# Performance work log

Measured on AMD Instinct MI355X. Metric: run time of the kernel, lower is better.

Reference implementation:

```python
import jax, jax.numpy as jnp
import numpy as np

D = 1024
H = 16
B = 8
N = 1024


def setup_inputs() -> dict:
    key = jax.random.key(0)
    k1, k2, k3 = jax.random.split(key, 3)
    x = jax.random.normal(k1, (B, N, D), dtype=jnp.float32)
    w_in = jax.random.normal(k2, (D, 3 * D), dtype=jnp.float32) * (1.0 / np.sqrt(D))
    w_out = jax.random.normal(k3, (D, D), dtype=jnp.float32) * (1.0 / np.sqrt(D))
    b_out = jnp.zeros((D,), dtype=jnp.float32)
    return {"x": x, "w_in": w_in, "w_out": w_out, "b_out": b_out}


def reference(x, w_in, w_out, b_out):
    h = H
    d = D // H
    scale = D ** (-0.5)  # note: full dimension, per source
    qkv = x @ w_in  # [B, N, 3D]
    # rearrange 'b n (qkv h d) -> qkv b h n d'
    qkv = qkv.reshape(x.shape[0], x.shape[1], 3, h, d)
    qkv = jnp.transpose(qkv, (2, 0, 3, 1, 4))
    q, k, v = qkv[0], qkv[1], qkv[2]
    scores = jnp.einsum('bhid,bhjd->bhij', q, k) * scale
    attn = jax.nn.softmax(scores, axis=-1)
    out = jnp.einsum('bhij,bhjd->bhid', attn, v)
    # 'b h n d -> b n (h d)'
    out = jnp.transpose(out, (0, 2, 1, 3)).reshape(x.shape[0], x.shape[1], h * d)
    return out @ w_out + b_out
```

## Files before the change

kernel.cpp:

```cpp
#include <hip/hip_runtime.h>
#include <stdint.h>
#include <stddef.h>

typedef __bf16 bf16;
typedef __bf16 bf16x4 __attribute__((ext_vector_type(4)));
typedef __bf16 bf16x8 __attribute__((ext_vector_type(8)));
typedef float  f32x4  __attribute__((ext_vector_type(4)));
typedef float  f32x16 __attribute__((ext_vector_type(16)));
typedef float  f32x4v __attribute__((ext_vector_type(4)));
typedef unsigned int u32x4 __attribute__((ext_vector_type(4)));

__device__ __forceinline__ void gload_lds16(const void* g, void* lds) {
  __builtin_amdgcn_global_load_lds(
      (__attribute__((address_space(1))) void*)(uintptr_t)g,
      (__attribute__((address_space(3))) void*)lds,
      16, 0, 0);
}

__device__ __forceinline__ unsigned int pk2(float a, float b) {
  unsigned short lo = __builtin_bit_cast(unsigned short, (bf16)a);
  unsigned short hi = __builtin_bit_cast(unsigned short, (bf16)b);
  return (unsigned int)lo | ((unsigned int)hi << 16);
}


__global__ void cvt_f32_to_bf16(const float* __restrict__ in, bf16* __restrict__ out, int n) {
  int i = (blockIdx.x * blockDim.x + threadIdx.x) * 4;
  if (i >= n) return;
  f32x4v v = *reinterpret_cast<const f32x4v*>(in + i);
  bf16x4 o;
  o[0] = (bf16)v[0]; o[1] = (bf16)v[1]; o[2] = (bf16)v[2]; o[3] = (bf16)v[3];
  *reinterpret_cast<bf16x4*>(out + i) = o;
}

__global__ void transpose_cvt(const float* __restrict__ in, bf16* __restrict__ out, int R, int C) {
  __shared__ bf16 tile[32][33];
  int c0 = blockIdx.x * 32, r0 = blockIdx.y * 32;
  int tx = threadIdx.x, ty = threadIdx.y;
  #pragma unroll
  for (int i = ty; i < 32; i += 8)
    tile[i][tx] = (bf16)in[(size_t)(r0 + i) * C + (c0 + tx)];
  __syncthreads();
  #pragma unroll
  for (int i = ty; i < 32; i += 8)
    out[(size_t)(c0 + i) * R + (r0 + tx)] = tile[tx][i];
}


template <typename OT, bool BIAS>
__global__ __launch_bounds__(256) void gemm_abt(
    const bf16* __restrict__ A,
    const bf16* __restrict__ Bt,
    const float* __restrict__ bias,
    OT* __restrict__ C, int M, int N, int K)
{
  __shared__ bf16 As[128 * 64];
  __shared__ bf16 Bs[128 * 64];

  const int tid = threadIdx.x;
  const int w = tid >> 6, l = tid & 63;
  const int l15 = l & 15, l4 = l >> 4, l7 = l & 7;
  const int wr = w >> 1, wc = w & 1;
  const int m0 = blockIdx.y * 128, n0 = blockIdx.x * 128;

  f32x4 acc[4][4];
  #pragma unroll
  for (int i = 0; i < 4; i++)
    #pragma unroll
    for (int j = 0; j < 4; j++) acc[i][j] = (f32x4){0.f, 0.f, 0.f, 0.f};

  const int srow  = w * 8 + (l >> 3);
  const int sslot = (l & 7) ^ ((l >> 3) & 7);
  const int KT = K >> 6;

  for (int kt = 0; kt < KT; ++kt) {
    __syncthreads();
    const int kcol = kt * 64 + sslot * 8;
    #pragma unroll
    for (int p = 0; p < 4; ++p) {
      gload_lds16(A  + (size_t)(m0 + p * 32 + srow) * K + kcol,
                  (char*)As + p * 4096 + w * 1024);
      gload_lds16(Bt + (size_t)(n0 + p * 32 + srow) * K + kcol,
                  (char*)Bs + p * 4096 + w * 1024);
    }
    __syncthreads();

    #pragma unroll
    for (int kk = 0; kk < 2; ++kk) {
      const int coff = (kk * 32 + l4 * 8) ^ (l7 << 3);
      bf16x8 af[4], bq[4];
      #pragma unroll
      for (int m = 0; m < 4; ++m) {
        int r = wr * 64 + m * 16 + l15;
        af[m] = *reinterpret_cast<const bf16x8*>(&As[r * 64 + coff]);
      }
      #pragma unroll
      for (int n = 0; n < 4; ++n) {
        int r = wc * 64 + n * 16 + l15;
        bq[n] = *reinterpret_cast<const bf16x8*>(&Bs[r * 64 + coff]);
      }
      #pragma unroll
      for (int m = 0; m < 4; ++m)
        #pragma unroll
        for (int n = 0; n < 4; ++n)
          acc[m][n] = __builtin_amdgcn_mfma_f32_16x16x32_bf16(af[m], bq[n], acc[m][n], 0, 0, 0);
    }
  }

  #pragma unroll
  for (int m = 0; m < 4; ++m) {
    #pragma unroll
    for (int n = 0; n < 4; ++n) {
      int col = n0 + wc * 64 + n * 16 + l15;
      float bv = BIAS ? bias[col] : 0.f;
      #pragma unroll
      for (int j = 0; j < 4; ++j) {
        int row = m0 + wr * 64 + m * 16 + l4 * 4 + j;
        float v = acc[m][n][j] + bv;
        C[(size_t)row * N + col] = (OT)v;
      }
    }
  }
}


__global__ __launch_bounds__(256) void attn_fused(
    const bf16* __restrict__ qkv,
    bf16* __restrict__ aout)
{
  __shared__ bf16 Ks[64 * 64];
  __shared__ bf16 Vt[64 * 64];

  const int tid = threadIdx.x;
  const int w = tid >> 6, l = tid & 63;
  const int l31 = l & 31, hi = l >> 5;

  const int bid = blockIdx.x;
  const int c  = bid & 7, rr = bid >> 3;
  const int g  = c * 16 + (rr & 15);
  const int qt = rr >> 4;
  const int h  = g & 15;
  const int b  = g >> 4;

  const bf16* base = qkv + (size_t)b * 1024 * 3072;
  const int qrow0 = qt * 128 + w * 32;

  const float qscale = 0.03125f * 1.44269504f;
  bf16x8 qf[4];
  #pragma unroll
  for (int st = 0; st < 4; st++) {
    const bf16* p = base + (size_t)(qrow0 + l31) * 3072 + h * 64 + st * 16 + hi * 8;
    bf16x8 v = *reinterpret_cast<const bf16x8*>(p);
    #pragma unroll
    for (int e = 0; e < 8; e++) v[e] = (bf16)((float)v[e] * qscale);
    qf[st] = v;
  }

  bf16x8 onesf;
  #pragma unroll
  for (int e = 0; e < 8; e++) onesf[e] = (bf16)1.0f;

  f32x16 acc0 = {}, acc1 = {}, accS = {};

  const int skey  = w * 8 + (l >> 3);
  const int sslot = (l & 7) ^ ((l >> 3) & 7);
  const int vd0   = (tid & 15) * 4;
  const int vk0   = (tid >> 4) * 4;
  const int vslot = tid >> 5;
  const int vhalf = (tid >> 4) & 1;

  for (int kt = 0; kt < 16; ++kt) {
    __syncthreads();
    #pragma unroll
    for (int p = 0; p < 2; ++p)
      gload_lds16(base + (size_t)(kt * 64 + p * 32 + skey) * 3072 + 1024 + h * 64 + sslot * 8,
                  (char*)Ks + p * 4096 + w * 1024);
    {
      bf16x4 vv[4];
      #pragma unroll
      for (int i = 0; i < 4; ++i)
        vv[i] = *reinterpret_cast<const bf16x4*>(
            base + (size_t)(kt * 64 + vk0 + i) * 3072 + 2048 + h * 64 + vd0);
      #pragma unroll
      for (int j = 0; j < 4; ++j) {
        int d = vd0 + j;
        bf16x4 o; o[0] = vv[0][j]; o[1] = vv[1][j]; o[2] = vv[2][j]; o[3] = vv[3][j];
        *reinterpret_cast<bf16x4*>(&Vt[d * 64 + ((vslot ^ (d & 7)) * 8 + vhalf * 4)]) = o;
      }
    }
    __syncthreads();

    #pragma unroll
    for (int ktile = 0; ktile < 2; ++ktile) {
      f32x16 s = {};
      const int key = ktile * 32 + l31;
      #pragma unroll
      for (int st = 0; st < 4; ++st) {
        const int slot = (2 * st + hi) ^ (key & 7);
        bf16x8 kf = *reinterpret_cast<const bf16x8*>(&Ks[key * 64 + slot * 8]);
        s = __builtin_amdgcn_mfma_f32_32x32x16_bf16(kf, qf[st], s, 0, 0, 0);
      }
      #pragma unroll
      for (int r = 0; r < 16; ++r) s[r] = exp2f(s[r]);
      u32x4 dw0 = {pk2(s[0], s[1]),  pk2(s[2], s[3]),
                   pk2(s[4], s[5]),  pk2(s[6], s[7])};
      u32x4 dw1 = {pk2(s[8], s[9]),  pk2(s[10], s[11]),
                   pk2(s[12], s[13]), pk2(s[14], s[15])};
      bf16x8 pf0 = __builtin_bit_cast(bf16x8, dw0);
      bf16x8 pf1 = __builtin_bit_cast(bf16x8, dw1);

      accS = __builtin_amdgcn_mfma_f32_32x32x16_bf16(pf0, onesf, accS, 0, 0, 0);
      accS = __builtin_amdgcn_mfma_f32_32x32x16_bf16(pf1, onesf, accS, 0, 0, 0);

      #pragma unroll
      for (int gg = 0; gg < 2; ++gg) {
        bf16x8 pf = gg ? pf1 : pf0;
        const int cb = ktile * 4 + gg * 2;
        const int d7 = l31 & 7;
        bf16x4 a0 = *reinterpret_cast<const bf16x4*>(
            &Vt[l31 * 64 + ((cb ^ d7) * 8 + hi * 4)]);
        bf16x4 b0 = *reinterpret_cast<const bf16x4*>(
            &Vt[l31 * 64 + (((cb + 1) ^ d7) * 8 + hi * 4)]);
        bf16x8 vf0;
        #pragma unroll
        for (int e = 0; e < 4; ++e) { vf0[e] = a0[e]; vf0[4 + e] = b0[e]; }
        acc0 = __builtin_amdgcn_mfma_f32_32x32x16_bf16(pf, vf0, acc0, 0, 0, 0);

        bf16x4 a1 = *reinterpret_cast<const bf16x4*>(
            &Vt[(32 + l31) * 64 + ((cb ^ d7) * 8 + hi * 4)]);
        bf16x4 b1 = *reinterpret_cast<const bf16x4*>(
            &Vt[(32 + l31) * 64 + (((cb + 1) ^ d7) * 8 + hi * 4)]);
        bf16x8 vf1;
        #pragma unroll
        for (int e = 0; e < 4; ++e) { vf1[e] = a1[e]; vf1[4 + e] = b1[e]; }
        acc1 = __builtin_amdgcn_mfma_f32_32x32x16_bf16(pf, vf1, acc1, 0, 0, 0);
      }
    }
  }

  #pragma unroll
  for (int reg = 0; reg < 16; ++reg) {
    int q_r = (reg & 3) + 8 * (reg >> 2) + 4 * hi;
    float rinv = 1.0f / accS[reg];
    size_t rowoff = ((size_t)b * 1024 + qrow0 + q_r) * 1024 + h * 64;
    aout[rowoff + l31]      = (bf16)(acc0[reg] * rinv);
    aout[rowoff + 32 + l31] = (bf16)(acc1[reg] * rinv);
  }
}


extern "C" void kernel_launch(void* const* d_in, const int* in_sizes, int n_in,
                              void* d_out, int out_size, void* d_ws, size_t ws_size,
                              hipStream_t stream) {
  const float* x     = (const float*)d_in[0];
  const float* w_in  = (const float*)d_in[1];
  const float* w_out = (const float*)d_in[2];
  const float* b_out = (const float*)d_in[3];
  float* out = (float*)d_out;

  bf16* xb    = (bf16*)d_ws;
  bf16* wint  = xb    + (size_t)8192 * 1024;
  bf16* woutt = wint  + (size_t)3072 * 1024;
  bf16* qkv   = woutt + (size_t)1024 * 1024;
  bf16* ao    = qkv   + (size_t)8192 * 3072;

  cvt_f32_to_bf16<<<8192, 256, 0, stream>>>(x, xb, 8192 * 1024);
  transpose_cvt<<<dim3(96, 32), dim3(32, 8), 0, stream>>>(w_in,  wint,  1024, 3072);
  transpose_cvt<<<dim3(32, 32), dim3(32, 8), 0, stream>>>(w_out, woutt, 1024, 1024);

  gemm_abt<bf16, false><<<dim3(24, 64), 256, 0, stream>>>(xb, wint, nullptr, qkv, 8192, 3072, 1024);

  attn_fused<<<1024, 256, 0, stream>>>(qkv, ao);

  gemm_abt<float, true><<<dim3(8, 64), 256, 0, stream>>>(ao, woutt, b_out, out, 8192, 1024, 1024);
}
```

Before: 188.8 us.

## Double-buffer K/V tiles in attention kernel and refine V swizzle

```diff
diff --git a/kernel.cpp b/kernel.cpp
--- a/kernel.cpp
+++ b/kernel.cpp
@@ -128,8 +128,8 @@
     const bf16* __restrict__ qkv,
     bf16* __restrict__ aout)
 {
-  __shared__ bf16 Ks[64 * 64];
-  __shared__ bf16 Vt[64 * 64];
+  __shared__ bf16 Ks[2][64 * 64];
+  __shared__ bf16 Vt[2][64 * 64];
 
   const int tid = threadIdx.x;
   const int w = tid >> 6, l = tid & 63;
@@ -169,26 +169,38 @@
   const int vslot = tid >> 5;
   const int vhalf = (tid >> 4) & 1;
 
+  bf16x4 vv[4];
+
+  #pragma unroll
+  for (int i = 0; i < 4; ++i)
+    vv[i] = *reinterpret_cast<const bf16x4*>(
+        base + (size_t)(vk0 + i) * 3072 + 2048 + h * 64 + vd0);
+  #pragma unroll
+  for (int p = 0; p < 2; ++p)
+    gload_lds16(base + (size_t)(p * 32 + skey) * 3072 + 1024 + h * 64 + sslot * 8,
+                (char*)Ks[0] + p * 4096 + w * 1024);
+  #pragma unroll
+  for (int j = 0; j < 4; ++j) {
+    int d = vd0 + j;
+    bf16x4 o; o[0] = vv[0][j]; o[1] = vv[1][j]; o[2] = vv[2][j]; o[3] = vv[3][j];
+    *reinterpret_cast<bf16x4*>(
+        &Vt[0][d * 64 + ((vslot ^ (d & 7) ^ ((d >> 3) & 7)) * 8 + vhalf * 4)]) = o;
+  }
+  __syncthreads();
+
   for (int kt = 0; kt < 16; ++kt) {
-    __syncthreads();
-    #pragma unroll
-    for (int p = 0; p < 2; ++p)
-      gload_lds16(base + (size_t)(kt * 64 + p * 32 + skey) * 3072 + 1024 + h * 64 + sslot * 8,
-                  (char*)Ks + p * 4096 + w * 1024);
-    {
-      bf16x4 vv[4];
+    const int cur = kt & 1, nxt = cur ^ 1;
+
+    if (kt < 15) {
       #pragma unroll
       for (int i = 0; i < 4; ++i)
         vv[i] = *reinterpret_cast<const bf16x4*>(
-            base + (size_t)(kt * 64 + vk0 + i) * 3072 + 2048 + h * 64 + vd0);
-      #pragma unroll
-      for (int j = 0; j < 4; ++j) {
-        int d = vd0 + j;
-        bf16x4 o; o[0] = vv[0][j]; o[1] = vv[1][j]; o[2] = vv[2][j]; o[3] = vv[3][j];
-        *reinterpret_cast<bf16x4*>(&Vt[d * 64 + ((vslot ^ (d & 7)) * 8 + vhalf * 4)]) = o;
-      }
-    }
-    __syncthreads();
+            base + (size_t)((kt + 1) * 64 + vk0 + i) * 3072 + 2048 + h * 64 + vd0);
+      #pragma unroll
+      for (int p = 0; p < 2; ++p)
+        gload_lds16(base + (size_t)((kt + 1) * 64 + p * 32 + skey) * 3072 + 1024 + h * 64 + sslot * 8,
+                    (char*)Ks[nxt] + p * 4096 + w * 1024);
+    }
 
     #pragma unroll
     for (int ktile = 0; ktile < 2; ++ktile) {
@@ -197,7 +209,7 @@
       #pragma unroll
       for (int st = 0; st < 4; ++st) {
         const int slot = (2 * st + hi) ^ (key & 7);
-        bf16x8 kf = *reinterpret_cast<const bf16x8*>(&Ks[key * 64 + slot * 8]);
+        bf16x8 kf = *reinterpret_cast<const bf16x8*>(&Ks[cur][key * 64 + slot * 8]);
         s = __builtin_amdgcn_mfma_f32_32x32x16_bf16(kf, qf[st], s, 0, 0, 0);
       }
       #pragma unroll
@@ -212,30 +224,42 @@
       accS = __builtin_amdgcn_mfma_f32_32x32x16_bf16(pf0, onesf, accS, 0, 0, 0);
       accS = __builtin_amdgcn_mfma_f32_32x32x16_bf16(pf1, onesf, accS, 0, 0, 0);
 
+      const int d7x0 = (l31 & 7) ^ (l31 >> 3);
+      const int d7x1 = d7x0 ^ 4;
       #pragma unroll
       for (int gg = 0; gg < 2; ++gg) {
         bf16x8 pf = gg ? pf1 : pf0;
         const int cb = ktile * 4 + gg * 2;
-        const int d7 = l31 & 7;
         bf16x4 a0 = *reinterpret_cast<const bf16x4*>(
-            &Vt[l31 * 64 + ((cb ^ d7) * 8 + hi * 4)]);
+            &Vt[cur][l31 * 64 + (((cb) ^ d7x0) * 8 + hi * 4)]);
         bf16x4 b0 = *reinterpret_cast<const bf16x4*>(
-            &Vt[l31 * 64 + (((cb + 1) ^ d7) * 8 + hi * 4)]);
+            &Vt[cur][l31 * 64 + (((cb + 1) ^ d7x0) * 8 + hi * 4)]);
         bf16x8 vf0;
         #pragma unroll
         for (int e = 0; e < 4; ++e) { vf0[e] = a0[e]; vf0[4 + e] = b0[e]; }
         acc0 = __builtin_amdgcn_mfma_f32_32x32x16_bf16(pf, vf0, acc0, 0, 0, 0);
 
         bf16x4 a1 = *reinterpret_cast<const bf16x4*>(
-            &Vt[(32 + l31) * 64 + ((cb ^ d7) * 8 + hi * 4)]);
+            &Vt[cur][(32 + l31) * 64 + (((cb) ^ d7x1) * 8 + hi * 4)]);
         bf16x4 b1 = *reinterpret_cast<const bf16x4*>(
-            &Vt[(32 + l31) * 64 + (((cb + 1) ^ d7) * 8 + hi * 4)]);
+            &Vt[cur][(32 + l31) * 64 + (((cb + 1) ^ d7x1) * 8 + hi * 4)]);
         bf16x8 vf1;
         #pragma unroll
         for (int e = 0; e < 4; ++e) { vf1[e] = a1[e]; vf1[4 + e] = b1[e]; }
         acc1 = __builtin_amdgcn_mfma_f32_32x32x16_bf16(pf, vf1, acc1, 0, 0, 0);
       }
     }
+
+    if (kt < 15) {
+      #pragma unroll
+      for (int j = 0; j < 4; ++j) {
+        int d = vd0 + j;
+        bf16x4 o; o[0] = vv[0][j]; o[1] = vv[1][j]; o[2] = vv[2][j]; o[3] = vv[3][j];
+        *reinterpret_cast<bf16x4*>(
+            &Vt[nxt][d * 64 + ((vslot ^ (d & 7) ^ ((d >> 3) & 7)) * 8 + vhalf * 4)]) = o;
+      }
+    }
+    __syncthreads();
   }
 
   #pragma unroll
```

Measured after the change: 192.7 us. +2.1%, slower.
